# Kernel tuning notes

Hardware: AMD Instinct MI355X
Metric: run time of the kernel (lower is better)

Reference implementation:

```python
import jax, jax.numpy as jnp
import numpy as np
import math

B, S, E_PHI, E_F, H_F, N_HEADS = 2, 2048, 1024, 1024, 1024, 16


def setup_inputs() -> dict:
    key = jax.random.key(0)
    ks = jax.random.split(key, 7)
    return {
        "q": jax.random.normal(ks[0], (B, S, E_PHI), dtype=jnp.float32),
        "k": jax.random.normal(ks[1], (B, S, E_PHI), dtype=jnp.float32),
        "v": jax.random.normal(ks[2], (B, S, E_F), dtype=jnp.float32),
        # weights stored as [in, out]; applied as x @ W (same math as nn.Linear with W^T)
        "W_q": jax.random.normal(ks[3], (E_PHI, H_F), dtype=jnp.float32) * 0.02,
        "W_k": jax.random.normal(ks[4], (E_PHI, H_F), dtype=jnp.float32) * 0.02,
        "W_v": jax.random.normal(ks[5], (E_F, H_F), dtype=jnp.float32) * 0.02,
        "W_o": jax.random.normal(ks[6], (H_F, E_F), dtype=jnp.float32) * 0.02,
    }


def reference(q, k, v, W_q, W_k, W_v, W_o):
    Bq, Sq, _ = q.shape
    Dh = H_F // N_HEADS
    scale = 1.0 / math.sqrt(H_F)
    # projections -> [B, H, S, Dh]
    qh = (q @ W_q).reshape(Bq, Sq, N_HEADS, Dh).transpose(0, 2, 1, 3)
    kh = (k @ W_k).reshape(Bq, Sq, N_HEADS, Dh).transpose(0, 2, 1, 3)
    vh = (v @ W_v).reshape(Bq, Sq, N_HEADS, Dh).transpose(0, 2, 1, 3)
    # near-causal mask: mask out j >= i (triu incl. diagonal), EXCEPT position [0,0]
    mask = jnp.triu(jnp.ones((Sq, Sq), dtype=bool), 0).at[0, 0].set(False)
    scores = jnp.einsum('bhsd,bhtd->bhst', qh, kh) * scale  # [B,H,S,S]
    scores = jnp.where(mask, -jnp.inf, scores)
    probs = jax.nn.softmax(scores, axis=-1)  # dropout = identity (eval mode)
    out = jnp.einsum('bhst,bhtd->bhsd', probs, vh)  # [B,H,S,Dh]
    out = out.transpose(0, 2, 1, 3).reshape(Bq, Sq, H_F)
    return out @ W_o
```

## Files before the change

kernel.cpp:

```cpp
#include <hip/hip_runtime.h>
#include <type_traits>

#define S_LEN 2048
#define NHEAD 16
#define DHEAD 64
#define EMB   1024
#define NBATCH 2

typedef __bf16 bf16_t;
typedef bf16_t bf16x8 __attribute__((ext_vector_type(8)));
typedef float  f32x4  __attribute__((ext_vector_type(4)));
typedef unsigned short us_t;
typedef us_t   us8    __attribute__((ext_vector_type(8)));
typedef us_t   us4    __attribute__((ext_vector_type(4)));
typedef unsigned int u32x4 __attribute__((ext_vector_type(4)));
typedef unsigned int u32x2 __attribute__((ext_vector_type(2)));
typedef short  s16x4  __attribute__((ext_vector_type(4)));

static __device__ __forceinline__ bf16x8 ld_bf16x8(const us_t* p) {
  return __builtin_bit_cast(bf16x8, *reinterpret_cast<const us8*>(p));
}
static __device__ __forceinline__ us_t f2bf(float f) {
  bf16_t h = (bf16_t)f;
  return __builtin_bit_cast(us_t, h);
}
static __device__ __forceinline__ unsigned cvt_pk_bf16(float lo, float hi) {
  unsigned r;
  asm("v_cvt_pk_bf16_f32 %0, %1, %2" : "=v"(r) : "v"(lo), "v"(hi));
  return r;
}
#if __has_builtin(__builtin_amdgcn_exp2f)
#define EXP2(x) __builtin_amdgcn_exp2f(x)
#else
#define EXP2(x) exp2f(x)
#endif
static __device__ __forceinline__ void gload16(const void* g, void* lds) {
  __builtin_amdgcn_global_load_lds((const __attribute__((address_space(1))) void*)g,
                                   (__attribute__((address_space(3))) void*)lds,
                                   16, 0, 0);
}

__global__ __launch_bounds__(256) void prep(const float* __restrict__ q,
                                            const float* __restrict__ k,
                                            const float* __restrict__ v,
                                            const float* __restrict__ W0,
                                            const float* __restrict__ W1,
                                            const float* __restrict__ W2,
                                            const float* __restrict__ W3,
                                            us_t* __restrict__ Qb,
                                            us_t* __restrict__ Kb,
                                            us_t* __restrict__ Vb,
                                            us_t* __restrict__ T0,
                                            us_t* __restrict__ T1,
                                            us_t* __restrict__ T2,
                                            us_t* __restrict__ T3) {
  const int z = blockIdx.z;
  if (z < 3) {
    const float* A = (z == 0) ? q : (z == 1) ? k : v;
    us_t* O = (z == 0) ? Qb : (z == 1) ? Kb : Vb;
    const int flat = blockIdx.y * 32 + blockIdx.x;
    const size_t i = ((size_t)flat * 256 + threadIdx.x) * 8;
    f32x4 lo = *reinterpret_cast<const f32x4*>(A + i);
    f32x4 hi = *reinterpret_cast<const f32x4*>(A + i + 4);
    us8 w;
#pragma unroll
    for (int j = 0; j < 4; ++j) { w[j] = f2bf(lo[j]); w[j + 4] = f2bf(hi[j]); }
    *reinterpret_cast<us8*>(O + i) = w;
  } else {
    if (blockIdx.y >= EMB / 32) return;
    __shared__ float tile[32][33];
    const int zz = z - 3;
    const float* W = (zz == 0) ? W0 : (zz == 1) ? W1 : (zz == 2) ? W2 : W3;
    us_t* WT = (zz == 0) ? T0 : (zz == 1) ? T1 : (zz == 2) ? T2 : T3;
    const int n0 = blockIdx.x * 32, k0 = blockIdx.y * 32;
    const int tx = threadIdx.x & 31, ty = threadIdx.x >> 5;
#pragma unroll
    for (int i = 0; i < 32; i += 8)
      tile[ty + i][tx] = W[(size_t)(k0 + ty + i) * EMB + n0 + tx];
    __syncthreads();
#pragma unroll
    for (int i = 0; i < 32; i += 8)
      WT[(size_t)(n0 + ty + i) * EMB + k0 + tx] = f2bf(tile[tx][ty + i]);
  }
}

template<int MODE>
static __device__ __forceinline__ void gemm_core(const us_t* __restrict__ A,
                                                 const us_t* __restrict__ BT,
                                                 void* __restrict__ O,
                                                 int mt, int nt,
                                                 char (*As)[8192], char (*Bs)[8192]) {
  const int lane = threadIdx.x & 63;
  const int wave = threadIdx.x >> 6;
  const int wm = (wave >> 1) * 64;
  const int wn = (wave & 1) * 64;
  const int lr = lane & 15;
  const int lg = lane >> 4;

  f32x4 acc[4][4] = {};

  auto stage = [&](int buf, int k0) {
#pragma unroll
    for (int i = 0; i < 2; ++i) {
      const int seg = wave * 2 + i;
      const int r = seg * 16 + (lane >> 2);
      const int cb = (lane & 3) * 16;
      gload16((const char*)A + ((size_t)(mt * 128 + r) * EMB + k0) * 2 + cb,
              &As[buf][seg * 1024]);
      gload16((const char*)BT + ((size_t)(nt * 128 + r) * EMB + k0) * 2 + cb,
              &Bs[buf][seg * 1024]);
    }
  };

  stage(0, 0);
  __syncthreads();

  for (int ks = 0; ks < EMB / 32; ++ks) {
    const int cur = ks & 1;
    if (ks + 1 < EMB / 32) stage(cur ^ 1, (ks + 1) * 32);
    bf16x8 af[4], bfr[4];
#pragma unroll
    for (int i = 0; i < 4; ++i)
      af[i] = ld_bf16x8((const us_t*)&As[cur][(wm + 16 * i + lr) * 64 + lg * 16]);
#pragma unroll
    for (int j = 0; j < 4; ++j)
      bfr[j] = ld_bf16x8((const us_t*)&Bs[cur][(wn + 16 * j + lr) * 64 + lg * 16]);
#pragma unroll
    for (int i = 0; i < 4; ++i)
#pragma unroll
      for (int j = 0; j < 4; ++j)
        acc[i][j] = __builtin_amdgcn_mfma_f32_16x16x32_bf16(af[i], bfr[j], acc[i][j], 0, 0, 0);
    __syncthreads();
  }

  const int crow = (lane >> 4) * 4;
#pragma unroll
  for (int i = 0; i < 4; ++i)
#pragma unroll
    for (int j = 0; j < 4; ++j)
#pragma unroll
      for (int r = 0; r < 4; ++r) {
        const int m = mt * 128 + wm + 16 * i + crow + r;
        const int n = nt * 128 + wn + 16 * j + lr;
        const float val = acc[i][j][r];
        if constexpr (MODE == 2) {
          ((float*)O)[(size_t)m * EMB + n] = val;
        } else {
          us_t* o = (us_t*)O;
          const int b = m >> 11, s = m & (S_LEN - 1);
          const int h = n >> 6, d = n & 63;
          if constexpr (MODE == 0)
            o[(((size_t)(b * NHEAD + h) * S_LEN + s) << 6) + d] = f2bf(val);
          else
            o[((size_t)(b * NHEAD + h) * DHEAD + d) * S_LEN + s] = f2bf(val);
        }
      }
}

__global__ __launch_bounds__(256) void proj3(const us_t* __restrict__ A0,
                                             const us_t* __restrict__ A1,
                                             const us_t* __restrict__ A2,
                                             const us_t* __restrict__ B0,
                                             const us_t* __restrict__ B1,
                                             const us_t* __restrict__ B2,
                                             us_t* __restrict__ O0,
                                             us_t* __restrict__ O1,
                                             us_t* __restrict__ O2) {
  __shared__ char As[2][8192];
  __shared__ char Bs[2][8192];
  const int f = blockIdx.x;
  const int w = (f & 7) * 96 + (f >> 3);
  const int z = w >> 8;
  const int rem = w & 255;
  const int mt = rem >> 3, nt = rem & 7;
  const us_t* A = (z == 0) ? A0 : (z == 1) ? A1 : A2;
  const us_t* BT = (z == 0) ? B0 : (z == 1) ? B1 : B2;
  us_t* O = (z == 0) ? O0 : (z == 1) ? O1 : O2;
  if (z < 2)
    gemm_core<0>(A, BT, O, mt, nt, As, Bs);
  else
    gemm_core<1>(A, BT, O, mt, nt, As, Bs);
}

__global__ __launch_bounds__(256) void gemmout(const us_t* __restrict__ A,
                                               const us_t* __restrict__ BT,
                                               float* __restrict__ O) {
  __shared__ char As[2][8192];
  __shared__ char Bs[2][8192];
  const int f = blockIdx.x;
  const int w = (f & 7) * 32 + (f >> 3);
  const int mt = w >> 3, nt = w & 7;
  gemm_core<2>(A, BT, O, mt, nt, As, Bs);
}

__global__ __launch_bounds__(256, 2) void attn128(const us_t* __restrict__ Qh,
                                                  const us_t* __restrict__ Kh,
                                                  const us_t* __restrict__ Vt,
                                                  us_t* __restrict__ AO) {
  __shared__ char Ks[2][8192];
  __shared__ char Vs[2][8192];
  const int flat = blockIdx.y * 32 + blockIdx.x;
  const int bh = (flat & 7) * 4 + ((flat >> 3) & 3);
  const int qt = 15 - (flat >> 5);
  const int lane = threadIdx.x & 63;
  const int wave = threadIdx.x >> 6;
  const int lr = lane & 15;
  const int lg = lane >> 4;
  const int qw = qt * 128 + wave * 32;
  const int qg[2] = { qw + lr, qw + 16 + lr };

  const us_t* qb0 = Qh + ((size_t)bh * S_LEN + qg[0]) * DHEAD;
  const us_t* qb1 = Qh + ((size_t)bh * S_LEN + qg[1]) * DHEAD;
  bf16x8 qf[2][2] = { { ld_bf16x8(qb0 + lg * 8), ld_bf16x8(qb0 + 32 + lg * 8) },
                      { ld_bf16x8(qb1 + lg * 8), ld_bf16x8(qb1 + 32 + lg * 8) } };

  const us_t* kbase0 = Kh + (size_t)bh * S_LEN * DHEAD;
  const us_t* vbase0 = Vt + (size_t)bh * DHEAD * S_LEN;

  int koff[8];
#pragma unroll
  for (int ks = 0; ks < 2; ++ks)
#pragma unroll
    for (int j = 0; j < 4; ++j)
      koff[ks * 4 + j] = (16 * j + lr) * 128 + ((ks * 64 + lg * 16) ^ ((lr & 7) << 4));
  int voff[16];
#pragma unroll
  for (int jk = 0; jk < 4; ++jk)
#pragma unroll
    for (int jd = 0; jd < 4; ++jd)
      voff[jk * 4 + jd] = (16 * jd + lr) * 128 + ((32 * jk + 8 * lg) ^ ((lr & 7) << 4));

  auto stage = [&](int buf, int t0) {
#pragma unroll
    for (int i = 0; i < 2; ++i) {
      const int seg = wave * 2 + i;
      const int r = seg * 8 + (lane >> 3);
      const int c16 = (lane & 7) ^ (lane >> 3);
      gload16(kbase0 + (size_t)(t0 + r) * DHEAD + c16 * 8, &Ks[buf][seg * 1024]);
      gload16(vbase0 + (size_t)r * S_LEN + t0 + c16 * 8, &Vs[buf][seg * 1024]);
    }
  };

  f32x4 oaccT[2][4] = {};
  float mrow[2] = { -1e9f, -1e9f };
  float lsum[2] = { 0.f, 0.f };
  const float c = 0.045084220f;

  stage(0, 0);
  __syncthreads();

  const int NT = 2 * qt + 2;
  for (int tt = 0; tt < NT; ++tt) {
    const int cur = tt & 1;
    if (tt + 1 < NT) stage(cur ^ 1, (tt + 1) * 64);
    const bool skip = (wave < 2) && (tt == NT - 1);
    if (!skip) {
      f32x4 sc[2][4] = {};
      __builtin_amdgcn_s_setprio(1);
#pragma unroll
      for (int ks = 0; ks < 2; ++ks)
#pragma unroll
        for (int j = 0; j < 4; ++j) {
          bf16x8 ak = ld_bf16x8((const us_t*)&Ks[cur][koff[ks * 4 + j]]);
          sc[0][j] = __builtin_amdgcn_mfma_f32_16x16x32_bf16(ak, qf[0][ks], sc[0][j], 0, 0, 0);
          sc[1][j] = __builtin_amdgcn_mfma_f32_16x16x32_bf16(ak, qf[1][ks], sc[1][j], 0, 0, 0);
        }
      __builtin_amdgcn_s_setprio(0);

      if (tt * 64 + 63 >= qw) {
#pragma unroll
        for (int qc = 0; qc < 2; ++qc)
#pragma unroll
          for (int j = 0; j < 4; ++j)
#pragma unroll
            for (int r = 0; r < 4; ++r) {
              const int t_g = tt * 64 + 16 * j + 4 * lg + r;
              const int qq = qg[qc];
              if (!((t_g < qq) || (qq == 0 && t_g == 0))) sc[qc][j][r] = -1e30f;
            }
      }

      unsigned int pk[2][4][2];
#pragma unroll
      for (int qc = 0; qc < 2; ++qc) {
        float mx = sc[qc][0][0];
#pragma unroll
        for (int j = 0; j < 4; ++j)
#pragma unroll
          for (int r = 0; r < 4; ++r) mx = fmaxf(mx, sc[qc][j][r]);
        const float mxc = mx * c;
        if (__any(mxc > mrow[qc] + 8.f)) {
          float mc = mxc;
          mc = fmaxf(mc, __shfl_xor(mc, 16, 64));
          mc = fmaxf(mc, __shfl_xor(mc, 32, 64));
          const float m2 = fmaxf(mrow[qc], mc);
          const float alpha = EXP2(mrow[qc] - m2);
          lsum[qc] *= alpha;
#pragma unroll
          for (int j = 0; j < 4; ++j)
#pragma unroll
            for (int r = 0; r < 4; ++r) oaccT[qc][j][r] *= alpha;
          mrow[qc] = m2;
        }
        float ps = 0.f;
#pragma unroll
        for (int j = 0; j < 4; ++j) {
          float p0 = EXP2(__builtin_fmaf(sc[qc][j][0], c, -mrow[qc]));
          float p1 = EXP2(__builtin_fmaf(sc[qc][j][1], c, -mrow[qc]));
          float p2 = EXP2(__builtin_fmaf(sc[qc][j][2], c, -mrow[qc]));
          float p3 = EXP2(__builtin_fmaf(sc[qc][j][3], c, -mrow[qc]));
          ps += (p0 + p1) + (p2 + p3);
          pk[qc][j][0] = cvt_pk_bf16(p0, p1);
          pk[qc][j][1] = cvt_pk_bf16(p2, p3);
        }
        lsum[qc] += ps;
      }

      __builtin_amdgcn_s_setprio(1);
#pragma unroll
      for (int jk = 0; jk < 4; ++jk) {
        s16x4 pf0 = __builtin_bit_cast(s16x4, (u32x2){pk[0][jk][0], pk[0][jk][1]});
        s16x4 pf1 = __builtin_bit_cast(s16x4, (u32x2){pk[1][jk][0], pk[1][jk][1]});
#pragma unroll
        for (int jd = 0; jd < 4; ++jd) {
          s16x4 av = __builtin_bit_cast(s16x4,
              *reinterpret_cast<const us4*>(&Vs[cur][voff[jk * 4 + jd]]));
          oaccT[0][jd] = __builtin_amdgcn_mfma_f32_16x16x16bf16_1k(av, pf0, oaccT[0][jd], 0, 0, 0);
          oaccT[1][jd] = __builtin_amdgcn_mfma_f32_16x16x16bf16_1k(av, pf1, oaccT[1][jd], 0, 0, 0);
        }
      }
      __builtin_amdgcn_s_setprio(0);
    }
    __syncthreads();
  }

  const int b = bh >> 4, h = bh & 15;
#pragma unroll
  for (int qc = 0; qc < 2; ++qc) {
    float ls = lsum[qc];
    ls += __shfl_xor(ls, 16, 64);
    ls += __shfl_xor(ls, 32, 64);
    const float inv = 1.0f / ls;
    us_t* aout = AO + (size_t)(b * S_LEN + qg[qc]) * EMB + h * DHEAD;
#pragma unroll
    for (int j = 0; j < 4; ++j) {
      us4 w;
#pragma unroll
      for (int r = 0; r < 4; ++r) w[r] = f2bf(oaccT[qc][j][r] * inv);
      *reinterpret_cast<us4*>(aout + 16 * j + 4 * lg) = w;
    }
  }
}

extern "C" void kernel_launch(void* const* d_in, const int* in_sizes, int n_in,
                              void* d_out, int out_size, void* d_ws, size_t ws_size,
                              hipStream_t stream) {
  const float* q  = (const float*)d_in[0];
  const float* k  = (const float*)d_in[1];
  const float* v  = (const float*)d_in[2];
  const float* Wq = (const float*)d_in[3];
  const float* Wk = (const float*)d_in[4];
  const float* Wv = (const float*)d_in[5];
  const float* Wo = (const float*)d_in[6];
  float* out = (float*)d_out;

  char* ws = (char*)d_ws;
  const size_t MB = 1024 * 1024;
  us_t* WqT = (us_t*)(ws + 0 * MB);
  us_t* WkT = (us_t*)(ws + 2 * MB);
  us_t* WvT = (us_t*)(ws + 4 * MB);
  us_t* WoT = (us_t*)(ws + 6 * MB);
  us_t* Qh  = (us_t*)(ws + 8 * MB);
  us_t* Kh  = (us_t*)(ws + 16 * MB);
  us_t* Vt  = (us_t*)(ws + 24 * MB);
  us_t* AO  = (us_t*)(ws + 32 * MB);
  us_t* Qb  = (us_t*)(ws + 32 * MB);
  us_t* Kb  = (us_t*)(ws + 40 * MB);
  us_t* Vb  = (us_t*)(ws + 48 * MB);

  prep<<<dim3(32, 64, 7), 256, 0, stream>>>(q, k, v, Wq, Wk, Wv, Wo,
                                            Qb, Kb, Vb, WqT, WkT, WvT, WoT);

  proj3<<<768, 256, 0, stream>>>(Qb, Kb, Vb, WqT, WkT, WvT, Qh, Kh, Vt);

  attn128<<<dim3(32, 16), 256, 0, stream>>>(Qh, Kh, Vt, AO);

  gemmout<<<256, 256, 0, stream>>>(AO, WoT, out);
}
```

Baseline: 139.4 us.

## Triple-buffer GEMM staging, vectorize conversions and V-transpose stores, reorder attention tiles

The GEMM core moves from two to three LDS buffers, keeping two global loads in flight. Each step now waits with a partial vmcnt and a raw s_barrier instead of a full __syncthreads. The fp32-to-bf16 cast uses packed conversions, and the transposed V projection writes four contiguous bf16 values per store. Attention query-tile order is interleaved heavy-first then light-first, which may balance causal work across the grid, while the larger LDS footprint may lower GEMM occupancy.

```diff
diff --git a/kernel.cpp b/kernel.cpp
--- a/kernel.cpp
+++ b/kernel.cpp
@@ -62,10 +62,9 @@
     const size_t i = ((size_t)flat * 256 + threadIdx.x) * 8;
     f32x4 lo = *reinterpret_cast<const f32x4*>(A + i);
     f32x4 hi = *reinterpret_cast<const f32x4*>(A + i + 4);
-    us8 w;
-#pragma unroll
-    for (int j = 0; j < 4; ++j) { w[j] = f2bf(lo[j]); w[j + 4] = f2bf(hi[j]); }
-    *reinterpret_cast<us8*>(O + i) = w;
+    u32x4 w = { cvt_pk_bf16(lo[0], lo[1]), cvt_pk_bf16(lo[2], lo[3]),
+                cvt_pk_bf16(hi[0], hi[1]), cvt_pk_bf16(hi[2], hi[3]) };
+    *reinterpret_cast<u32x4*>(O + i) = w;
   } else {
     if (blockIdx.y >= EMB / 32) return;
     __shared__ float tile[32][33];
@@ -96,6 +95,7 @@
   const int wn = (wave & 1) * 64;
   const int lr = lane & 15;
   const int lg = lane >> 4;
+  constexpr int NK = EMB / 32;
 
   f32x4 acc[4][4] = {};
 
@@ -111,50 +111,69 @@
               &Bs[buf][seg * 1024]);
     }
   };
-
-  stage(0, 0);
-  __syncthreads();
-
-  for (int ks = 0; ks < EMB / 32; ++ks) {
-    const int cur = ks & 1;
-    if (ks + 1 < EMB / 32) stage(cur ^ 1, (ks + 1) * 32);
+  auto mfma_step = [&](int buf) {
     bf16x8 af[4], bfr[4];
 #pragma unroll
     for (int i = 0; i < 4; ++i)
-      af[i] = ld_bf16x8((const us_t*)&As[cur][(wm + 16 * i + lr) * 64 + lg * 16]);
+      af[i] = ld_bf16x8((const us_t*)&As[buf][(wm + 16 * i + lr) * 64 + lg * 16]);
 #pragma unroll
     for (int j = 0; j < 4; ++j)
-      bfr[j] = ld_bf16x8((const us_t*)&Bs[cur][(wn + 16 * j + lr) * 64 + lg * 16]);
+      bfr[j] = ld_bf16x8((const us_t*)&Bs[buf][(wn + 16 * j + lr) * 64 + lg * 16]);
 #pragma unroll
     for (int i = 0; i < 4; ++i)
 #pragma unroll
       for (int j = 0; j < 4; ++j)
         acc[i][j] = __builtin_amdgcn_mfma_f32_16x16x32_bf16(af[i], bfr[j], acc[i][j], 0, 0, 0);
-    __syncthreads();
+  };
+
+  stage(0, 0);
+  stage(1, 32);
+  asm volatile("s_waitcnt vmcnt(4)" ::: "memory");
+  __builtin_amdgcn_s_barrier();
+
+  for (int ks = 0; ks < NK; ++ks) {
+    const int cur = ks % 3;
+    if (ks + 2 < NK) stage((ks + 2) % 3, (ks + 2) * 32);
+    mfma_step(cur);
+    if (ks + 1 < NK) {
+      if (ks + 2 < NK) asm volatile("s_waitcnt vmcnt(4)" ::: "memory");
+      else             asm volatile("s_waitcnt vmcnt(0)" ::: "memory");
+      __builtin_amdgcn_s_barrier();
+    }
   }
 
   const int crow = (lane >> 4) * 4;
 #pragma unroll
   for (int i = 0; i < 4; ++i)
 #pragma unroll
-    for (int j = 0; j < 4; ++j)
-#pragma unroll
-      for (int r = 0; r < 4; ++r) {
-        const int m = mt * 128 + wm + 16 * i + crow + r;
+    for (int j = 0; j < 4; ++j) {
+      if constexpr (MODE == 1) {
+        const int m = mt * 128 + wm + 16 * i + crow;
         const int n = nt * 128 + wn + 16 * j + lr;
-        const float val = acc[i][j][r];
-        if constexpr (MODE == 2) {
-          ((float*)O)[(size_t)m * EMB + n] = val;
-        } else {
-          us_t* o = (us_t*)O;
-          const int b = m >> 11, s = m & (S_LEN - 1);
-          const int h = n >> 6, d = n & 63;
-          if constexpr (MODE == 0)
+        const int b = m >> 11, s = m & (S_LEN - 1);
+        const int h = n >> 6, d = n & 63;
+        us4 w;
+#pragma unroll
+        for (int r = 0; r < 4; ++r) w[r] = f2bf(acc[i][j][r]);
+        *reinterpret_cast<us4*>((us_t*)O +
+            ((size_t)(b * NHEAD + h) * DHEAD + d) * S_LEN + s) = w;
+      } else {
+#pragma unroll
+        for (int r = 0; r < 4; ++r) {
+          const int m = mt * 128 + wm + 16 * i + crow + r;
+          const int n = nt * 128 + wn + 16 * j + lr;
+          const float val = acc[i][j][r];
+          if constexpr (MODE == 2) {
+            ((float*)O)[(size_t)m * EMB + n] = val;
+          } else {
+            us_t* o = (us_t*)O;
+            const int b = m >> 11, s = m & (S_LEN - 1);
+            const int h = n >> 6, d = n & 63;
             o[(((size_t)(b * NHEAD + h) * S_LEN + s) << 6) + d] = f2bf(val);
-          else
-            o[((size_t)(b * NHEAD + h) * DHEAD + d) * S_LEN + s] = f2bf(val);
+          }
         }
       }
+    }
 }
 
 __global__ __launch_bounds__(256) void proj3(const us_t* __restrict__ A0,
@@ -166,8 +185,8 @@
                                              us_t* __restrict__ O0,
                                              us_t* __restrict__ O1,
                                              us_t* __restrict__ O2) {
-  __shared__ char As[2][8192];
-  __shared__ char Bs[2][8192];
+  __shared__ char As[3][8192];
+  __shared__ char Bs[3][8192];
   const int f = blockIdx.x;
   const int w = (f & 7) * 96 + (f >> 3);
   const int z = w >> 8;
@@ -185,8 +204,8 @@
 __global__ __launch_bounds__(256) void gemmout(const us_t* __restrict__ A,
                                                const us_t* __restrict__ BT,
                                                float* __restrict__ O) {
-  __shared__ char As[2][8192];
-  __shared__ char Bs[2][8192];
+  __shared__ char As[3][8192];
+  __shared__ char Bs[3][8192];
   const int f = blockIdx.x;
   const int w = (f & 7) * 32 + (f >> 3);
   const int mt = w >> 3, nt = w & 7;
@@ -201,7 +220,8 @@
   __shared__ char Vs[2][8192];
   const int flat = blockIdx.y * 32 + blockIdx.x;
   const int bh = (flat & 7) * 4 + ((flat >> 3) & 3);
-  const int qt = 15 - (flat >> 5);
+  const int g = flat >> 5;
+  const int qt = (g >> 3) ? (g & 7) : 15 - (g & 7);
   const int lane = threadIdx.x & 63;
   const int wave = threadIdx.x >> 6;
   const int lr = lane & 15;
```

After: 136.0 us. 2.5% less time.
